# Performance work log

Measured on AMD Instinct MI355X. Metric: run time of the kernel, lower is better.

Reference implementation:

```python
import jax, jax.numpy as jnp
import numpy as np

N, F, H, G = 8192, 128, 64, 4      # nodes, node_attr_size, hidden_size, num groups
CONV_TH = 1e-05
MAX_ITER = 5


def setup_inputs() -> dict:
    key = jax.random.key(0)
    k1, k2, k3, k4 = jax.random.split(key, 4)
    X = jax.random.normal(k1, (N, F), dtype=jnp.float32)
    # L scaled like a normalized graph operator so the fixed-point is well-behaved
    L = jax.random.normal(k2, (N, N), dtype=jnp.float32) * (1.0 / np.sqrt(N))
    # reservoir weights (requires_grad=False in the original, still materialized here)
    W_ih = jax.random.normal(k3, (G, H, F), dtype=jnp.float32) * (1.0 / np.sqrt(F))
    W_hh = jax.random.normal(k4, (G, H, H), dtype=jnp.float32) * (0.9 / np.sqrt(H))
    return {"X": X, "L": L, "W_ih": W_ih, "W_hh": W_hh}


def _gesn_forward(X, L, W_ih, W_hh):
    # wiu = linear(X, W_ih) per group: [G, N, H]
    wiu = jnp.einsum('nf,ghf->gnh', X, W_ih)
    hx0 = jnp.zeros((G, N, H), dtype=X.dtype)
    done0 = jnp.zeros((G,), dtype=bool)

    def step(carry, _):
        hx, done = carry
        lin = jnp.einsum('gnh,gkh->gnk', hx, W_hh)          # linear(hx, W_hh)
        new = jnp.tanh(wiu + jnp.einsum('nm,gmk->gnk', L, lin))  # mm(L, .) + wiu, tanh activation
        diff = jnp.sqrt(jnp.sum((new - hx) ** 2, axis=(1, 2)))   # ||last_res - res|| per group
        hx_next = jnp.where(done[:, None, None], hx, new)   # masked early-exit (mimics break)
        done = done | (diff < CONV_TH)
        return (hx_next, done), None

    (hx, _), _ = jax.lax.scan(step, (hx0, done0), None, length=MAX_ITER)
    # concat group outputs along feature dim -> [N, G*H]
    return jnp.transpose(hx, (1, 0, 2)).reshape(N, G * H)


def reference(X, L, W_ih, W_hh):
    return _gesn_forward(X, L, W_ih, W_hh)
```

## Files before the change

kernel.cpp:

```cpp
#include <hip/hip_runtime.h>
#include <hip/hip_fp16.h>

#define NN 8192
#define FF 128
#define HH 64
#define GG 4
#define CONV_TH2 1e-10f

typedef _Float16 half8 __attribute__((ext_vector_type(8)));
typedef float floatx4 __attribute__((ext_vector_type(4)));

#define OFF_WIU  134217728ull
#define OFF_LIN  142606336ull
#define OFF_CP   146800640ull
#define OFF_META 180355072ull

__device__ __forceinline__ void load16(const void* g, void* l) {
  __builtin_amdgcn_global_load_lds((const __attribute__((address_space(1))) void*)g,
                                   (__attribute__((address_space(3))) void*)l,
                                   16, 0, 0);
}

__global__ void k_init(float* __restrict__ diffsq, int* __restrict__ done) {
  int t = threadIdx.x;
  if (t < 5 * GG) diffsq[t] = 0.f;
  if (t < GG) done[t] = 0;
}

__global__ void k_done(const float* __restrict__ diffsq, int* __restrict__ done, int it) {
  int t = threadIdx.x;
  if (t < GG) {
    if (diffsq[it * GG + t] < CONV_TH2) done[t] = 1;
  }
}

__global__ __launch_bounds__(256) void k_convert(const float* __restrict__ L,
                                                 _Float16* __restrict__ Lh) {
  size_t i = ((size_t)blockIdx.x * 256 + threadIdx.x) * 8;
  float4 a = *(const float4*)(L + i);
  float4 b = *(const float4*)(L + i + 4);
  half8 h;
  h[0] = (_Float16)a.x; h[1] = (_Float16)a.y; h[2] = (_Float16)a.z; h[3] = (_Float16)a.w;
  h[4] = (_Float16)b.x; h[5] = (_Float16)b.y; h[6] = (_Float16)b.z; h[7] = (_Float16)b.w;
  *(half8*)(Lh + i) = h;
}

__global__ __launch_bounds__(256) void k_wiu(const float* __restrict__ X,
    const float* __restrict__ Wih, const float* __restrict__ Whh,
    float* __restrict__ wiu, float* __restrict__ hx,
    _Float16* __restrict__ lin_t, float* __restrict__ diffsq) {
  __shared__ __align__(16) float smem[2 * 64 * 128];
  float* Xs = smem;
  float* Ws = smem + 64 * 128;
  const int bx = blockIdx.x, g = blockIdx.y;
  const int t = threadIdx.x;
  const int m0 = bx * 64;
  #pragma unroll
  for (int p = 0; p < 8; ++p) {
    int idx = p * 256 + t;
    int row = idx >> 5;
    int c4 = idx & 31;
    int sw = (c4 ^ (row >> 2)) & 31;
    float4 xv = *(const float4*)(X + (size_t)(m0 + row) * FF + c4 * 4);
    *(float4*)(Xs + row * 128 + sw * 4) = xv;
    float4 wv = *(const float4*)(Wih + (size_t)g * HH * FF + (size_t)row * FF + c4 * 4);
    *(float4*)(Ws + row * 128 + sw * 4) = wv;
  }
  __syncthreads();
  const int tc = t & 15, tm = t >> 4;
  float acc[4][4];
  #pragma unroll
  for (int r = 0; r < 4; ++r)
    #pragma unroll
    for (int s = 0; s < 4; ++s) acc[r][s] = 0.f;
  for (int f4 = 0; f4 < 32; ++f4) {
    float4 xv[4], wv[4];
    #pragma unroll
    for (int r = 0; r < 4; ++r) {
      int m = tm * 4 + r;
      xv[r] = *(const float4*)(Xs + m * 128 + (((f4 ^ (m >> 2)) & 31) * 4));
    }
    #pragma unroll
    for (int s = 0; s < 4; ++s) {
      int c = tc * 4 + s;
      wv[s] = *(const float4*)(Ws + c * 128 + (((f4 ^ (c >> 2)) & 31) * 4));
    }
    #pragma unroll
    for (int r = 0; r < 4; ++r)
      #pragma unroll
      for (int s = 0; s < 4; ++s)
        acc[r][s] += xv[r].x * wv[s].x + xv[r].y * wv[s].y +
                     xv[r].z * wv[s].z + xv[r].w * wv[s].w;
  }
  __syncthreads();
  float* hxs = smem;
  float* Whs = smem + 64 * 65;
  float diffp = 0.f;
  #pragma unroll
  for (int r = 0; r < 4; ++r) {
    int ml = tm * 4 + r;
    size_t off = (size_t)(m0 + ml) * 256 + g * 64 + tc * 4;
    float4 wv = make_float4(acc[r][0], acc[r][1], acc[r][2], acc[r][3]);
    *(float4*)(wiu + off) = wv;
    float4 hv;
    hv.x = tanhf(wv.x); hv.y = tanhf(wv.y); hv.z = tanhf(wv.z); hv.w = tanhf(wv.w);
    *(float4*)(hx + off) = hv;
    hxs[ml * 65 + tc * 4 + 0] = hv.x;
    hxs[ml * 65 + tc * 4 + 1] = hv.y;
    hxs[ml * 65 + tc * 4 + 2] = hv.z;
    hxs[ml * 65 + tc * 4 + 3] = hv.w;
    diffp += hv.x * hv.x + hv.y * hv.y + hv.z * hv.z + hv.w * hv.w;
  }
  #pragma unroll
  for (int p = 0; p < 16; ++p) {
    int idx = p * 256 + t;
    Whs[(idx >> 6) * 65 + (idx & 63)] = Whh[(size_t)g * HH * HH + idx];
  }
  for (int o = 32; o; o >>= 1) diffp += __shfl_down(diffp, o);
  if ((t & 63) == 0) atomicAdd(diffsq + g, diffp);
  __syncthreads();
  const int ml = t & 63, wv_ = t >> 6;
  float lacc[16];
  #pragma unroll
  for (int i = 0; i < 16; ++i) lacc[i] = 0.f;
  for (int h = 0; h < 64; ++h) {
    float xh = hxs[ml * 65 + h];
    #pragma unroll
    for (int i = 0; i < 16; ++i)
      lacc[i] += xh * Whs[(wv_ + 4 * i) * 65 + h];
  }
  #pragma unroll
  for (int i = 0; i < 16; ++i)
    lin_t[(size_t)(g * 64 + wv_ + 4 * i) * NN + m0 + ml] = (_Float16)lacc[i];
}

__global__ __launch_bounds__(256) void k_gemm(const _Float16* __restrict__ A,
    const _Float16* __restrict__ Bt, float* __restrict__ Cp) {
  __shared__ __align__(16) _Float16 As[128 * 64];
  __shared__ __align__(16) _Float16 Bs[128 * 64];
  const int bx = blockIdx.x;
  const int by = blockIdx.y;
  const int bz = blockIdx.z;
  const int t = threadIdx.x;
  const int lane = t & 63, wid = t >> 6;
  const int wr = wid >> 1, wc = wid & 1;
  const int l15 = lane & 15, quad = lane >> 4;
  const size_t m0 = (size_t)bx * 128;
  const size_t c0 = (size_t)by * 128;
  const size_t k0 = (size_t)bz * 2048;

  const _Float16* ga[4]; const _Float16* gb[4];
  _Float16* la[4]; _Float16* lb[4];
  #pragma unroll
  for (int i = 0; i < 4; ++i) {
    int ch = i * 256 + t;
    int r = ch >> 3;
    int j = (ch & 7) ^ (r & 7);
    ga[i] = A + (m0 + r) * NN + k0 + j * 8;
    gb[i] = Bt + (c0 + r) * NN + k0 + j * 8;
    la[i] = &As[ch * 8];
    lb[i] = &Bs[ch * 8];
  }
  int aoffs[2][4], boffs[2][4];
  #pragma unroll
  for (int ks = 0; ks < 2; ++ks) {
    #pragma unroll
    for (int mt = 0; mt < 4; ++mt) {
      int m = wr * 64 + mt * 16 + l15;
      aoffs[ks][mt] = m * 64 + (((ks * 4 + quad) ^ (m & 7)) * 8);
    }
    #pragma unroll
    for (int nt = 0; nt < 4; ++nt) {
      int n = wc * 64 + nt * 16 + l15;
      boffs[ks][nt] = n * 64 + (((ks * 4 + quad) ^ (n & 7)) * 8);
    }
  }
  floatx4 acc[4][4];
  #pragma unroll
  for (int mt = 0; mt < 4; ++mt)
    #pragma unroll
    for (int nt = 0; nt < 4; ++nt)
      acc[mt][nt] = (floatx4){0.f, 0.f, 0.f, 0.f};

  for (int rd = 0; rd < 32; ++rd) {
    #pragma unroll
    for (int i = 0; i < 4; ++i) { load16(ga[i], la[i]); load16(gb[i], lb[i]); }
    __syncthreads();
    #pragma unroll
    for (int ks = 0; ks < 2; ++ks) {
      half8 af[4], bf[4];
      #pragma unroll
      for (int mt = 0; mt < 4; ++mt) af[mt] = *(const half8*)&As[aoffs[ks][mt]];
      #pragma unroll
      for (int nt = 0; nt < 4; ++nt) bf[nt] = *(const half8*)&Bs[boffs[ks][nt]];
      #pragma unroll
      for (int mt = 0; mt < 4; ++mt)
        #pragma unroll
        for (int nt = 0; nt < 4; ++nt)
          acc[mt][nt] = __builtin_amdgcn_mfma_f32_16x16x32_f16(af[mt], bf[nt], acc[mt][nt], 0, 0, 0);
    }
    __syncthreads();
    #pragma unroll
    for (int i = 0; i < 4; ++i) { ga[i] += 64; gb[i] += 64; }
  }
  float* Cb = Cp + (size_t)bz * NN * 256;
  #pragma unroll
  for (int mt = 0; mt < 4; ++mt) {
    #pragma unroll
    for (int nt = 0; nt < 4; ++nt) {
      size_t gm = m0 + wr * 64 + mt * 16 + quad * 4;
      size_t gc = c0 + wc * 64 + nt * 16 + l15;
      #pragma unroll
      for (int rg = 0; rg < 4; ++rg)
        Cb[(gm + rg) * 256 + gc] = acc[mt][nt][rg];
    }
  }
}

__global__ __launch_bounds__(256) void k_post(const float* __restrict__ Cp,
    const float* __restrict__ wiu, const float* __restrict__ Whh,
    float* __restrict__ hx, _Float16* __restrict__ lin_t,
    float* __restrict__ diffsq, const int* __restrict__ done,
    int it, int write_lin) {
  __shared__ float hxs[64 * 65];
  __shared__ float Whs[64 * 65];
  const int bx = blockIdx.x, g = blockIdx.y, t = threadIdx.x;
  const int m0 = bx * 64;
  const int tcol = t & 15, trow = t >> 4;
  const int dn = done[g];
  float diffp = 0.f;
  #pragma unroll
  for (int p = 0; p < 4; ++p) {
    int ml = p * 16 + trow;
    size_t off = (size_t)(m0 + ml) * 256 + g * 64 + tcol * 4;
    float4 s  = *(const float4*)(Cp + off);
    float4 q1 = *(const float4*)(Cp + (size_t)1 * NN * 256 + off);
    float4 q2 = *(const float4*)(Cp + (size_t)2 * NN * 256 + off);
    float4 q3 = *(const float4*)(Cp + (size_t)3 * NN * 256 + off);
    s.x += q1.x + q2.x + q3.x; s.y += q1.y + q2.y + q3.y;
    s.z += q1.z + q2.z + q3.z; s.w += q1.w + q2.w + q3.w;
    float4 wv = *(const float4*)(wiu + off);
    float4 old = *(const float4*)(hx + off);
    float4 nv;
    nv.x = tanhf(wv.x + s.x); nv.y = tanhf(wv.y + s.y);
    nv.z = tanhf(wv.z + s.z); nv.w = tanhf(wv.w + s.w);
    float4 ov;
    ov.x = dn ? old.x : nv.x; ov.y = dn ? old.y : nv.y;
    ov.z = dn ? old.z : nv.z; ov.w = dn ? old.w : nv.w;
    *(float4*)(hx + off) = ov;
    float dx = nv.x - old.x, dy = nv.y - old.y, dz = nv.z - old.z, dw = nv.w - old.w;
    diffp += dx * dx + dy * dy + dz * dz + dw * dw;
    hxs[ml * 65 + tcol * 4 + 0] = ov.x;
    hxs[ml * 65 + tcol * 4 + 1] = ov.y;
    hxs[ml * 65 + tcol * 4 + 2] = ov.z;
    hxs[ml * 65 + tcol * 4 + 3] = ov.w;
  }
  if (write_lin) {
    #pragma unroll
    for (int p = 0; p < 16; ++p) {
      int idx = p * 256 + t;
      Whs[(idx >> 6) * 65 + (idx & 63)] = Whh[(size_t)g * HH * HH + idx];
    }
  }
  for (int o = 32; o; o >>= 1) diffp += __shfl_down(diffp, o);
  if ((t & 63) == 0) atomicAdd(diffsq + it * GG + g, diffp);
  if (!write_lin) return;
  __syncthreads();
  const int ml = t & 63, wv_ = t >> 6;
  float lacc[16];
  #pragma unroll
  for (int i = 0; i < 16; ++i) lacc[i] = 0.f;
  for (int h = 0; h < 64; ++h) {
    float xh = hxs[ml * 65 + h];
    #pragma unroll
    for (int i = 0; i < 16; ++i)
      lacc[i] += xh * Whs[(wv_ + 4 * i) * 65 + h];
  }
  #pragma unroll
  for (int i = 0; i < 16; ++i)
    lin_t[(size_t)(g * 64 + wv_ + 4 * i) * NN + m0 + ml] = (_Float16)lacc[i];
}

extern "C" void kernel_launch(void* const* d_in, const int* in_sizes, int n_in,
                              void* d_out, int out_size, void* d_ws, size_t ws_size,
                              hipStream_t stream) {
  const float* X   = (const float*)d_in[0];
  const float* L   = (const float*)d_in[1];
  const float* Wih = (const float*)d_in[2];
  const float* Whh = (const float*)d_in[3];
  float* out = (float*)d_out;
  char* ws = (char*)d_ws;
  _Float16* Lh    = (_Float16*)ws;
  float*    wiu   = (float*)(ws + OFF_WIU);
  _Float16* lin_t = (_Float16*)(ws + OFF_LIN);
  float*    Cp    = (float*)(ws + OFF_CP);
  float*    diffsq = (float*)(ws + OFF_META);
  int*      done   = (int*)(ws + OFF_META + 128);

  k_init<<<1, 64, 0, stream>>>(diffsq, done);
  k_convert<<<32768, 256, 0, stream>>>(L, Lh);
  k_wiu<<<dim3(128, 4), 256, 0, stream>>>(X, Wih, Whh, wiu, out, lin_t, diffsq);
  k_done<<<1, 64, 0, stream>>>(diffsq, done, 0);
  for (int it = 1; it <= 4; ++it) {
    k_gemm<<<dim3(64, 2, 4), 256, 0, stream>>>(Lh, lin_t, Cp);
    k_post<<<dim3(128, 4), 256, 0, stream>>>(Cp, wiu, Whh, out, lin_t, diffsq, done,
                                             it, (it < 4) ? 1 : 0);
    k_done<<<1, 64, 0, stream>>>(diffsq, done, it);
  }
}
```

Measured before the change: 761.9 us.

## Double-buffer GEMM LDS staging and fold convergence checks into post kernel

The GEMM kernel now uses two LDS buffers, issuing the global-to-LDS loads for the next K-slice before computing on the current one. This hides load latency behind MFMA work and drops one barrier per step. Separately, the init and done kernels are removed: diffsq is zeroed inside k_convert, and each k_post recomputes the done flag from the earlier diffsq entries, which saves about six small launches. The cost is doubled LDS use (64KB per block), which may lower occupancy.

```diff
diff --git a/kernel.cpp b/kernel.cpp
--- a/kernel.cpp
+++ b/kernel.cpp
@@ -21,21 +21,10 @@
                                    16, 0, 0);
 }
 
-__global__ void k_init(float* __restrict__ diffsq, int* __restrict__ done) {
-  int t = threadIdx.x;
-  if (t < 5 * GG) diffsq[t] = 0.f;
-  if (t < GG) done[t] = 0;
-}
-
-__global__ void k_done(const float* __restrict__ diffsq, int* __restrict__ done, int it) {
-  int t = threadIdx.x;
-  if (t < GG) {
-    if (diffsq[it * GG + t] < CONV_TH2) done[t] = 1;
-  }
-}
-
 __global__ __launch_bounds__(256) void k_convert(const float* __restrict__ L,
-                                                 _Float16* __restrict__ Lh) {
+                                                 _Float16* __restrict__ Lh,
+                                                 float* __restrict__ diffsq) {
+  if (blockIdx.x == 0 && threadIdx.x < 32) diffsq[threadIdx.x] = 0.f;
   size_t i = ((size_t)blockIdx.x * 256 + threadIdx.x) * 8;
   float4 a = *(const float4*)(L + i);
   float4 b = *(const float4*)(L + i + 4);
@@ -134,10 +123,36 @@
     lin_t[(size_t)(g * 64 + wv_ + 4 * i) * NN + m0 + ml] = (_Float16)lacc[i];
 }
 
+
+__device__ __forceinline__ void g_stage(const _Float16* ga, const _Float16* gb,
+                                        _Float16* lbase) {
+  #pragma unroll
+  for (int i = 0; i < 4; ++i) {
+    load16(ga + (size_t)i * 32 * NN, lbase + i * 2048);
+    load16(gb + (size_t)i * 32 * NN, lbase + 8192 + i * 2048);
+  }
+}
+
+__device__ __forceinline__ void g_compute(const _Float16* sbase,
+    const int (&aoffs)[2][4], const int (&boffs)[2][4], floatx4 (&acc)[4][4]) {
+  #pragma unroll
+  for (int ks = 0; ks < 2; ++ks) {
+    half8 af[4], bf[4];
+    #pragma unroll
+    for (int mt = 0; mt < 4; ++mt) af[mt] = *(const half8*)(sbase + aoffs[ks][mt]);
+    #pragma unroll
+    for (int nt = 0; nt < 4; ++nt) bf[nt] = *(const half8*)(sbase + 8192 + boffs[ks][nt]);
+    #pragma unroll
+    for (int mt = 0; mt < 4; ++mt)
+      #pragma unroll
+      for (int nt = 0; nt < 4; ++nt)
+        acc[mt][nt] = __builtin_amdgcn_mfma_f32_16x16x32_f16(af[mt], bf[nt], acc[mt][nt], 0, 0, 0);
+  }
+}
+
 __global__ __launch_bounds__(256) void k_gemm(const _Float16* __restrict__ A,
     const _Float16* __restrict__ Bt, float* __restrict__ Cp) {
-  __shared__ __align__(16) _Float16 As[128 * 64];
-  __shared__ __align__(16) _Float16 Bs[128 * 64];
+  __shared__ __align__(16) _Float16 smem[32768];
   const int bx = blockIdx.x;
   const int by = blockIdx.y;
   const int bz = blockIdx.z;
@@ -149,18 +164,12 @@
   const size_t c0 = (size_t)by * 128;
   const size_t k0 = (size_t)bz * 2048;
 
-  const _Float16* ga[4]; const _Float16* gb[4];
-  _Float16* la[4]; _Float16* lb[4];
-  #pragma unroll
-  for (int i = 0; i < 4; ++i) {
-    int ch = i * 256 + t;
-    int r = ch >> 3;
-    int j = (ch & 7) ^ (r & 7);
-    ga[i] = A + (m0 + r) * NN + k0 + j * 8;
-    gb[i] = Bt + (c0 + r) * NN + k0 + j * 8;
-    la[i] = &As[ch * 8];
-    lb[i] = &Bs[ch * 8];
-  }
+  const int r_ = t >> 3;
+  const int j_ = (t & 7) ^ (r_ & 7);
+  const _Float16* ga = A  + (m0 + r_) * NN + k0 + (size_t)j_ * 8;
+  const _Float16* gb = Bt + (c0 + r_) * NN + k0 + (size_t)j_ * 8;
+  _Float16* lb = &smem[t * 8];
+
   int aoffs[2][4], boffs[2][4];
   #pragma unroll
   for (int ks = 0; ks < 2; ++ks) {
@@ -182,27 +191,21 @@
     for (int nt = 0; nt < 4; ++nt)
       acc[mt][nt] = (floatx4){0.f, 0.f, 0.f, 0.f};
 
-  for (int rd = 0; rd < 32; ++rd) {
-    #pragma unroll
-    for (int i = 0; i < 4; ++i) { load16(ga[i], la[i]); load16(gb[i], lb[i]); }
+  g_stage(ga, gb, lb); ga += 64; gb += 64;
+  __syncthreads();
+  for (int it2 = 0; it2 < 15; ++it2) {
+    g_stage(ga, gb, lb + 16384); ga += 64; gb += 64;
+    g_compute(smem, aoffs, boffs, acc);
     __syncthreads();
-    #pragma unroll
-    for (int ks = 0; ks < 2; ++ks) {
-      half8 af[4], bf[4];
-      #pragma unroll
-      for (int mt = 0; mt < 4; ++mt) af[mt] = *(const half8*)&As[aoffs[ks][mt]];
-      #pragma unroll
-      for (int nt = 0; nt < 4; ++nt) bf[nt] = *(const half8*)&Bs[boffs[ks][nt]];
-      #pragma unroll
-      for (int mt = 0; mt < 4; ++mt)
-        #pragma unroll
-        for (int nt = 0; nt < 4; ++nt)
-          acc[mt][nt] = __builtin_amdgcn_mfma_f32_16x16x32_f16(af[mt], bf[nt], acc[mt][nt], 0, 0, 0);
-    }
+    g_stage(ga, gb, lb); ga += 64; gb += 64;
+    g_compute(smem + 16384, aoffs, boffs, acc);
     __syncthreads();
-    #pragma unroll
-    for (int i = 0; i < 4; ++i) { ga[i] += 64; gb[i] += 64; }
-  }
+  }
+  g_stage(ga, gb, lb + 16384);
+  g_compute(smem, aoffs, boffs, acc);
+  __syncthreads();
+  g_compute(smem + 16384, aoffs, boffs, acc);
+
   float* Cb = Cp + (size_t)bz * NN * 256;
   #pragma unroll
   for (int mt = 0; mt < 4; ++mt) {
@@ -220,14 +223,16 @@
 __global__ __launch_bounds__(256) void k_post(const float* __restrict__ Cp,
     const float* __restrict__ wiu, const float* __restrict__ Whh,
     float* __restrict__ hx, _Float16* __restrict__ lin_t,
-    float* __restrict__ diffsq, const int* __restrict__ done,
-    int it, int write_lin) {
+    float* __restrict__ diffsq, int it, int write_lin) {
   __shared__ float hxs[64 * 65];
   __shared__ float Whs[64 * 65];
   const int bx = blockIdx.x, g = blockIdx.y, t = threadIdx.x;
   const int m0 = bx * 64;
   const int tcol = t & 15, trow = t >> 4;
-  const int dn = done[g];
+  int dn = 0;
+  #pragma unroll
+  for (int j = 0; j < 4; ++j)
+    if (j < it) dn |= (diffsq[j * GG + g] < CONV_TH2) ? 1 : 0;
   float diffp = 0.f;
   #pragma unroll
   for (int p = 0; p < 4; ++p) {
@@ -295,16 +300,12 @@
   _Float16* lin_t = (_Float16*)(ws + OFF_LIN);
   float*    Cp    = (float*)(ws + OFF_CP);
   float*    diffsq = (float*)(ws + OFF_META);
-  int*      done   = (int*)(ws + OFF_META + 128);
-
-  k_init<<<1, 64, 0, stream>>>(diffsq, done);
-  k_convert<<<32768, 256, 0, stream>>>(L, Lh);
+
+  k_convert<<<32768, 256, 0, stream>>>(L, Lh, diffsq);
   k_wiu<<<dim3(128, 4), 256, 0, stream>>>(X, Wih, Whh, wiu, out, lin_t, diffsq);
-  k_done<<<1, 64, 0, stream>>>(diffsq, done, 0);
   for (int it = 1; it <= 4; ++it) {
     k_gemm<<<dim3(64, 2, 4), 256, 0, stream>>>(Lh, lin_t, Cp);
-    k_post<<<dim3(128, 4), 256, 0, stream>>>(Cp, wiu, Whh, out, lin_t, diffsq, done,
+    k_post<<<dim3(128, 4), 256, 0, stream>>>(Cp, wiu, Whh, out, lin_t, diffsq,
                                              it, (it < 4) ? 1 : 0);
-    k_done<<<1, 64, 0, stream>>>(diffsq, done, it);
-  }
-}
+  }
+}
```

After: 740.8 us. 2.8% less time.
